# Optimization experiments

Measured on AMD Instinct MI355X. Metric: run time of the kernel, lower is better.

## Reference

```python
import jax, jax.numpy as jnp
import numpy as np

MAGBIAS = 0.01
INV_SQRT2 = np.float32(1.0 / np.sqrt(2.0))


def _reflect(x, minx, maxx):
    # Half-sample symmetric reflection of indices (static numpy; matches dtcwt reflect()).
    rng = maxx - minx
    mod = np.fmod(x - minx, 2.0 * rng)
    mod = np.where(mod < 0, mod + 2.0 * rng, mod)
    out = np.where(mod >= rng, 2.0 * rng - mod, mod) + minx
    return np.round(out).astype(np.int64)


def _symm_pad(l, m):
    return _reflect(np.arange(-m, l + m, dtype=np.float64), -0.5, l - 0.5)


def _depthwise(X, h, axis, stride):
    # Per-channel 1-D correlation along rows (axis=2) or cols (axis=3), NCHW, like F.conv2d(groups=ch).
    ch = X.shape[1]
    if axis == 2:
        k = h.reshape(1, 1, -1, 1)
        strides = (stride, 1)
    else:
        k = h.reshape(1, 1, 1, -1)
        strides = (1, stride)
    k = jnp.tile(k, (ch, 1, 1, 1)).astype(X.dtype)
    return jax.lax.conv_general_dilated(
        X, k, window_strides=strides, padding='VALID',
        dimension_numbers=('NCHW', 'OIHW', 'NCHW'), feature_group_count=ch)


def colfilter(X, h):
    m = h.shape[0] // 2
    xe = _symm_pad(X.shape[2], m)
    return _depthwise(X[:, :, xe, :], h, axis=2, stride=1)


def rowfilter(X, h):
    m = h.shape[0] // 2
    xe = _symm_pad(X.shape[3], m)
    return _depthwise(X[:, :, :, xe], h, axis=3, stride=1)


def coldfilt(X, ha, hb, highpass):
    # Dual-tree decimated column filtering with a quarter-shift pair; output rows = r // 2.
    b, ch, r, c = X.shape
    m = ha.shape[0]
    xe = _symm_pad(r, m)
    ya = _depthwise(X[:, :, xe[2::2], :], ha, axis=2, stride=2)  # (b,ch,r/4,c)
    yb = _depthwise(X[:, :, xe[3::2], :], hb, axis=2, stride=2)
    first, second = (yb, ya) if highpass else (ya, yb)
    return jnp.stack([first, second], axis=3).reshape(b, ch, r // 2, c)


def rowdfilt(X, ha, hb, highpass):
    b, ch, r, c = X.shape
    m = ha.shape[0]
    xe = _symm_pad(c, m)
    ya = _depthwise(X[:, :, :, xe[2::2]], ha, axis=3, stride=2)
    yb = _depthwise(X[:, :, :, xe[3::2]], hb, axis=3, stride=2)
    first, second = (yb, ya) if highpass else (ya, yb)
    return jnp.stack([first, second], axis=4).reshape(b, ch, r, c // 2)


def q2c(y):
    # Quads -> two complex subbands (real, imag): the DTCWT butterfly combine.
    y = y * INV_SQRT2
    a = y[..., 0::2, 0::2]
    b = y[..., 0::2, 1::2]
    c = y[..., 1::2, 0::2]
    d = y[..., 1::2, 1::2]
    return (a - d, b + c), (a + d, b - c)


def _stack_orients(lh, hl, hh):
    (d15r, d15i), (d165r, d165i) = q2c(lh)
    (d45r, d45i), (d135r, d135i) = q2c(hh)
    (d75r, d75i), (d105r, d105i) = q2c(hl)
    reals = jnp.stack([d15r, d45r, d75r, d105r, d135r, d165r], axis=1)
    imags = jnp.stack([d15i, d45i, d75i, d105i, d135i, d165i], axis=1)
    return reals, imags


def fwd_j1(x, h0, h1):
    # Level-1 DTCWT: undecimated separable biorthogonal filters + q2c.
    lo = rowfilter(x, h0)
    hi = rowfilter(x, h1)
    ll = colfilter(lo, h0)
    lh = colfilter(lo, h1)
    hl = colfilter(hi, h0)
    hh = colfilter(hi, h1)
    reals, imags = _stack_orients(lh, hl, hh)
    return ll, reals, imags


def fwd_j2plus(x, h0a, h1a, h0b, h1b):
    # Level-2 DTCWT: decimated quarter-shift filter pairs + q2c.
    lo = rowdfilt(x, h0b, h0a, False)
    hi = rowdfilt(x, h1b, h1a, True)
    ll = coldfilt(lo, h0b, h0a, False)
    lh = coldfilt(lo, h1b, h1a, True)
    hl = coldfilt(hi, h0b, h0a, False)
    hh = coldfilt(hi, h1b, h1a, True)
    reals, imags = _stack_orients(lh, hl, hh)
    return ll, reals, imags


def _smooth_mag(re, im, bias):
    return jnp.sqrt(re * re + im * im + bias * bias) - bias


def _avgpool2(x):
    b, ch, r, c = x.shape
    return x.reshape(b, ch, r // 2, 2, c // 2, 2).mean(axis=(3, 5))


def _scat_forward(x, h0o, h1o, h0a, h0b, h1a, h1b):
    b, ch, r, c = x.shape  # r, c multiples of 8 (input already padded)
    # First order, scale j=1
    ll, re, im = fwd_j1(x, h0o, h1o)
    s1_j1 = _smooth_mag(re, im, MAGBIAS)                      # (b,6,ch,r/2,c/2)
    # First order, scale j=2 (on the running lowpass)
    ll, re, im = fwd_j2plus(ll, h0a, h1a, h0b, h1b)           # ll: (b,ch,r/2,c/2)
    s1_j2 = _smooth_mag(re, im, MAGBIAS)                      # (b,6,ch,r/4,c/4)
    # Second order: one more octave on the first-order magnitudes
    p = s1_j1.reshape(b, 6 * ch, r // 2, c // 2)
    p, re, im = fwd_j1(p, h0o, h1o)
    s2 = _smooth_mag(re, im, MAGBIAS).reshape(b, 36, ch, r // 4, c // 4)
    s0 = _avgpool2(ll)[:, None]                               # (b,1,ch,r/4,c/4)
    s1_j1 = _avgpool2(p).reshape(b, 6, ch, r // 4, c // 4)
    Z = jnp.concatenate([s0, s1_j1, s1_j2, s2], axis=1)       # (b,49,ch,r/4,c/4)
    return Z.reshape(b, 49 * ch, r // 4, c // 4)


def setup_inputs():
    key = jax.random.key(0)
    ks = jax.random.split(key, 5)
    x = jax.random.normal(ks[0], (32, 3, 512, 512), dtype=jnp.float32)
    h0o = jax.random.normal(ks[1], (5,), dtype=jnp.float32) * 0.3
    h1o = jax.random.normal(ks[2], (7,), dtype=jnp.float32) * 0.3
    h0a = jax.random.normal(ks[3], (10,), dtype=jnp.float32) * 0.3
    h1a = jax.random.normal(ks[4], (10,), dtype=jnp.float32) * 0.3
    h0b = h0a[::-1]  # quarter-shift pair: time-reverse of the tree-a filter
    h1b = h1a[::-1]
    return {"x": x, "h0o": h0o, "h1o": h1o, "h0a": h0a, "h0b": h0b,
            "h1a": h1a, "h1b": h1b}


def reference(x, h0o, h1o, h0a, h0b, h1a, h1b):
    return _scat_forward(x, h0o, h1o, h0a, h0b, h1a, h1b)
```

## Files before the change

kernel.cpp:

```cpp
#include <hip/hip_runtime.h>

#define IS2 0.70710678118654752440f

__device__ __forceinline__ int refl(int i, int n) {
    if (i < 0) i = -1 - i;
    if (i >= n) i = 2 * n - 1 - i;
    return i;
}

__device__ __forceinline__ float smag(float re, float im) {
    return sqrtf(re * re + im * im + 1.0e-4f) - 0.01f;
}

template <int MODE>
__global__ __launch_bounds__(256, 4)
void fwd_j1_kernel(const float* __restrict__ in,
                   const float* __restrict__ h0,
                   const float* __restrict__ h1,
                   float* __restrict__ ll_out,
                   float* __restrict__ mag_out,
                   int CH, int N)
{
    const int img = blockIdx.z;
    const int b   = img / CH;
    const int chn = img % CH;
    const int ty0 = blockIdx.y * 64;
    const int tx0 = blockIdx.x * 64;
    const int tid = threadIdx.x;

    __shared__ __align__(16) float sx[70 * 72];
    __shared__ __align__(16) float slo[70 * 64];
    float* const shi = sx;

    float f0[5], f1[7];
#pragma unroll
    for (int t = 0; t < 5; ++t) f0[t] = h0[t];
#pragma unroll
    for (int t = 0; t < 7; ++t) f1[t] = h1[t];

    const float* src = in + (size_t)img * N * N;

    for (int e = tid; e < 70 * 70; e += 256) {
        int rr = e / 70, cc = e % 70;
        int gr = refl(ty0 - 3 + rr, N);
        int gc = refl(tx0 - 3 + cc, N);
        sx[rr * 72 + cc] = src[(size_t)gr * N + gc];
    }
    __syncthreads();

    float rlo[5][4], rhi[5][4];
#pragma unroll
    for (int k = 0; k < 5; ++k) {
        int e = tid + k * 256;
        if (e < 1120) {
            int rr = e >> 4, g = e & 15;
            const float4* w4 = (const float4*)&sx[rr * 72 + 4 * g];
            float4 wa = w4[0], wb = w4[1], wc = w4[2];
            float win[12] = {wa.x, wa.y, wa.z, wa.w,
                             wb.x, wb.y, wb.z, wb.w,
                             wc.x, wc.y, wc.z, wc.w};
#pragma unroll
            for (int u = 0; u < 4; ++u) {
                float lo = 0.f, hi = 0.f;
#pragma unroll
                for (int t = 0; t < 5; ++t) lo += win[u + 1 + t] * f0[t];
#pragma unroll
                for (int t = 0; t < 7; ++t) hi += win[u + t] * f1[t];
                rlo[k][u] = lo; rhi[k][u] = hi;
            }
        }
    }
    __syncthreads();
#pragma unroll
    for (int k = 0; k < 5; ++k) {
        int e = tid + k * 256;
        if (e < 1120) {
            int rr = e >> 4, g = e & 15;
            *(float4*)&slo[rr * 64 + 4 * g] =
                make_float4(rlo[k][0], rlo[k][1], rlo[k][2], rlo[k][3]);
            *(float4*)&shi[rr * 64 + 4 * g] =
                make_float4(rhi[k][0], rhi[k][1], rhi[k][2], rhi[k][3]);
        }
    }
    __syncthreads();

    const int j     = tid & 63;
    const int rg    = tid >> 6;
    const int rbase = rg * 16;

    float clo[22], chi[22];
#pragma unroll
    for (int t = 0; t < 22; ++t) {
        clo[t] = slo[(rbase + t) * 64 + j];
        chi[t] = shi[(rbase + t) * 64 + j];
    }

    const int Nh  = N >> 1;
    const int par = j & 1;
    const int qx  = (tx0 >> 1) + (j >> 1);
    const int qy0 = (ty0 >> 1) + rg * 8;
    const int oLH = par ? 5 : 0;
    const int oHH = par ? 4 : 1;
    const int oHL = par ? 3 : 2;

    float* lcol = nullptr;
    float* pLH = nullptr; float* pHH = nullptr; float* pHL = nullptr;
    float* zBase = nullptr;
    size_t zLH = 0, zHH = 0, zHL = 0, zPL = 0;
    if (MODE == 0) {
        lcol = ll_out + (size_t)img * N * N + (size_t)(ty0 + rbase) * N + tx0 + j;
        const size_t planeSz = (size_t)Nh * Nh;
        const size_t qoff = (size_t)qy0 * Nh + qx;
        pLH = mag_out + ((size_t)(b * 6 + oLH) * CH + chn) * planeSz + qoff;
        pHH = mag_out + ((size_t)(b * 6 + oHH) * CH + chn) * planeSz + qoff;
        pHL = mag_out + ((size_t)(b * 6 + oHL) * CH + chn) * planeSz + qoff;
    } else {
        const int o1 = chn / 3, c3 = chn % 3;
        zBase = mag_out + (size_t)b * 147 * 16384 + (size_t)qy0 * 128 + qx;
        zLH = (size_t)((13 + oLH * 6 + o1) * 3 + c3) * 16384;
        zHH = (size_t)((13 + oHH * 6 + o1) * 3 + c3) * 16384;
        zHL = (size_t)((13 + oHL * 6 + o1) * 3 + c3) * 16384;
        zPL = (size_t)((1 + o1) * 3 + c3) * 16384;
    }

#pragma unroll
    for (int ii = 0; ii < 8; ++ii) {
        const int i0 = 2 * ii, i1 = 2 * ii + 1;
        float ll0 = 0.f, ll1 = 0.f, lh0 = 0.f, lh1 = 0.f;
        float hl0 = 0.f, hl1 = 0.f, hh0 = 0.f, hh1 = 0.f;
#pragma unroll
        for (int t = 0; t < 5; ++t) {
            ll0 += clo[i0 + 1 + t] * f0[t]; ll1 += clo[i1 + 1 + t] * f0[t];
            hl0 += chi[i0 + 1 + t] * f0[t]; hl1 += chi[i1 + 1 + t] * f0[t];
        }
#pragma unroll
        for (int t = 0; t < 7; ++t) {
            lh0 += clo[i0 + t] * f1[t]; lh1 += clo[i1 + t] * f1[t];
            hh0 += chi[i0 + t] * f1[t]; hh1 += chi[i1 + t] * f1[t];
        }

        float lhT = __shfl_xor(lh0, 1), lhB = __shfl_xor(lh1, 1);
        float hhT = __shfl_xor(hh0, 1), hhB = __shfl_xor(hh1, 1);
        float hlT = __shfl_xor(hl0, 1), hlB = __shfl_xor(hl1, 1);
        float mLH = smag(IS2 * (lh0 - lhB), IS2 * (lhT + lh1));
        float mHH = smag(IS2 * (hh0 - hhB), IS2 * (hhT + hh1));
        float mHL = smag(IS2 * (hl0 - hlB), IS2 * (hlT + hl1));

        if (MODE == 0) {
            lcol[(size_t)i0 * N] = ll0;
            lcol[(size_t)i1 * N] = ll1;
            pLH[(size_t)ii * Nh] = mLH;
            pHH[(size_t)ii * Nh] = mHH;
            pHL[(size_t)ii * Nh] = mHL;
        } else {
            float* zr = zBase + (size_t)ii * 128;
            zr[zLH] = mLH;
            zr[zHH] = mHH;
            zr[zHL] = mHL;
            float llT = __shfl_xor(ll0, 1), llB = __shfl_xor(ll1, 1);
            if (par == 0) {
                zr[zPL] = 0.25f * (ll0 + ll1 + llT + llB);
            }
        }
    }
}

__global__ __launch_bounds__(256, 4)
void fwd_j2_kernel(const float* __restrict__ ll,
                   const float* __restrict__ h0a, const float* __restrict__ h0b,
                   const float* __restrict__ h1a, const float* __restrict__ h1b,
                   float* __restrict__ Z)
{
    const int img = blockIdx.z;
    const int b = img / 3, c = img % 3;
    const int r0 = blockIdx.y * 32;
    const int c0 = blockIdx.x * 32;
    const int tid = threadIdx.x;

    __shared__ float sx[80 * 84];
    float* const sloP = sx;
    float* const shiP = sx + 2688;

    float fa0[10], fb0[10], fa1[10], fb1[10];
#pragma unroll
    for (int t = 0; t < 10; ++t) {
        fa0[t] = h0a[t]; fb0[t] = h0b[t];
        fa1[t] = h1a[t]; fb1[t] = h1b[t];
    }

    const float* src = ll + (size_t)img * 512 * 512;

    for (int e = tid; e < 80 * 80; e += 256) {
        int rr = e / 80, cc = e % 80;
        int gr = refl(2 * r0 - 8 + rr, 512);
        int gc = refl(2 * c0 - 8 + cc, 512);
        sx[rr * 84 + cc] = src[(size_t)gr * 512 + gc];
    }
    __syncthreads();

    const int jj  = tid & 31;
    const int odd = jj & 1;
    const int base = 2 * (jj & ~1);
    float hlo[10], hhi[10];
#pragma unroll
    for (int t = 0; t < 10; ++t) {
        hlo[t] = odd ? fa0[t] : fb0[t];
        hhi[t] = odd ? fb1[t] : fa1[t];
    }
    const int offlo = base + odd;
    const int offhi = base + 1 - odd;
    float rlo[10], rhi[10];
#pragma unroll
    for (int k = 0; k < 10; ++k) {
        int rr = (tid >> 5) + 8 * k;
        const float* row = &sx[rr * 84];
        float lo = 0.f, hi = 0.f;
#pragma unroll
        for (int t = 0; t < 10; ++t) {
            lo += row[offlo + 2 * t] * hlo[t];
            hi += row[offhi + 2 * t] * hhi[t];
        }
        rlo[k] = lo; rhi[k] = hi;
    }
    __syncthreads();
#pragma unroll
    for (int k = 0; k < 10; ++k) {
        int rr = (tid >> 5) + 8 * k;
        sloP[rr * 33 + jj] = rlo[k];
        shiP[rr * 33 + jj] = rhi[k];
    }
    __syncthreads();

    const int qi = tid >> 4, qj = tid & 15;
    float ll2[2][2], lh4[2][2], hl4[2][2], hh4[2][2];
#pragma unroll
    for (int dj = 0; dj < 2; ++dj) {
        const int col = 2 * qj + dj;
        const int rb  = 4 * qi;
        float vll0 = 0.f, vll1 = 0.f, vlh0 = 0.f, vlh1 = 0.f;
        float vhl0 = 0.f, vhl1 = 0.f, vhh0 = 0.f, vhh1 = 0.f;
#pragma unroll
        for (int t = 0; t < 10; ++t) {
            float e0 = sloP[(rb + 2 * t) * 33 + col];
            float e1 = sloP[(rb + 2 * t + 1) * 33 + col];
            float g0 = shiP[(rb + 2 * t) * 33 + col];
            float g1 = shiP[(rb + 2 * t + 1) * 33 + col];
            vll0 += e0 * fb0[t];
            vll1 += e1 * fa0[t];
            vlh0 += e1 * fa1[t];
            vlh1 += e0 * fb1[t];
            vhl0 += g0 * fb0[t];
            vhl1 += g1 * fa0[t];
            vhh0 += g1 * fa1[t];
            vhh1 += g0 * fb1[t];
        }
        ll2[0][dj] = vll0; ll2[1][dj] = vll1;
        lh4[0][dj] = vlh0; lh4[1][dj] = vlh1;
        hl4[0][dj] = vhl0; hl4[1][dj] = vhl1;
        hh4[0][dj] = vhh0; hh4[1][dj] = vhh1;
    }

    const int qy = (r0 >> 1) + qi;
    const int qx = (c0 >> 1) + qj;
    float* Zb = Z + (size_t)b * 147 * 16384 + (size_t)qy * 128 + qx;

    Zb[(size_t)c * 16384] =
        0.25f * (ll2[0][0] + ll2[0][1] + ll2[1][0] + ll2[1][1]);

    {
        float a, bq, cq, d;
        float m[6];
        a = lh4[0][0] * IS2; bq = lh4[0][1] * IS2; cq = lh4[1][0] * IS2; d = lh4[1][1] * IS2;
        m[0] = smag(a - d, bq + cq); m[5] = smag(a + d, bq - cq);
        a = hh4[0][0] * IS2; bq = hh4[0][1] * IS2; cq = hh4[1][0] * IS2; d = hh4[1][1] * IS2;
        m[1] = smag(a - d, bq + cq); m[4] = smag(a + d, bq - cq);
        a = hl4[0][0] * IS2; bq = hl4[0][1] * IS2; cq = hl4[1][0] * IS2; d = hl4[1][1] * IS2;
        m[2] = smag(a - d, bq + cq); m[3] = smag(a + d, bq - cq);
#pragma unroll
        for (int o = 0; o < 6; ++o) {
            Zb[(size_t)((7 + o) * 3 + c) * 16384] = m[o];
        }
    }
}

extern "C" void kernel_launch(void* const* d_in, const int* in_sizes, int n_in,
                              void* d_out, int out_size, void* d_ws, size_t ws_size,
                              hipStream_t stream)
{
    const float* x   = (const float*)d_in[0];
    const float* h0o = (const float*)d_in[1];
    const float* h1o = (const float*)d_in[2];
    const float* h0a = (const float*)d_in[3];
    const float* h0b = (const float*)d_in[4];
    const float* h1a = (const float*)d_in[5];
    const float* h1b = (const float*)d_in[6];
    float* Z = (float*)d_out;

    float* ws_ll = (float*)d_ws;
    float* ws_p  = ws_ll + (size_t)32 * 3 * 512 * 512;

    dim3 blk(256);
    fwd_j1_kernel<0><<<dim3(8, 8, 96), blk, 0, stream>>>(x, h0o, h1o, ws_ll, ws_p, 3, 512);
    fwd_j2_kernel<<<dim3(8, 8, 96), blk, 0, stream>>>(ws_ll, h0a, h0b, h1a, h1b, Z);
    fwd_j1_kernel<1><<<dim3(4, 4, 576), blk, 0, stream>>>(ws_p, h0o, h1o, nullptr, Z, 18, 256);
}
```

Baseline: 630.3 us.

## Merge second-level and j1-on-magnitudes kernels into one launch

```diff
diff --git a/kernel.cpp b/kernel.cpp
--- a/kernel.cpp
+++ b/kernel.cpp
@@ -13,23 +13,21 @@
 }
 
 template <int MODE>
-__global__ __launch_bounds__(256, 4)
-void fwd_j1_kernel(const float* __restrict__ in,
-                   const float* __restrict__ h0,
-                   const float* __restrict__ h1,
-                   float* __restrict__ ll_out,
-                   float* __restrict__ mag_out,
-                   int CH, int N)
-{
-    const int img = blockIdx.z;
+__device__ __forceinline__
+void j1_tile(float* __restrict__ smem,
+             const float* __restrict__ in,
+             const float* __restrict__ h0,
+             const float* __restrict__ h1,
+             float* __restrict__ ll_out,
+             float* __restrict__ mag_out,
+             int CH, int N, int img, int ty0, int tx0)
+{
     const int b   = img / CH;
     const int chn = img % CH;
-    const int ty0 = blockIdx.y * 64;
-    const int tx0 = blockIdx.x * 64;
     const int tid = threadIdx.x;
 
-    __shared__ __align__(16) float sx[70 * 72];
-    __shared__ __align__(16) float slo[70 * 64];
+    float* const sx  = smem;
+    float* const slo = smem + 5040;
     float* const shi = sx;
 
     float f0[5], f1[7];
@@ -165,19 +163,17 @@
     }
 }
 
-__global__ __launch_bounds__(256, 4)
-void fwd_j2_kernel(const float* __restrict__ ll,
-                   const float* __restrict__ h0a, const float* __restrict__ h0b,
-                   const float* __restrict__ h1a, const float* __restrict__ h1b,
-                   float* __restrict__ Z)
-{
-    const int img = blockIdx.z;
+__device__ __forceinline__
+void j2_tile(float* __restrict__ smem,
+             const float* __restrict__ ll,
+             const float* __restrict__ h0a, const float* __restrict__ h0b,
+             const float* __restrict__ h1a, const float* __restrict__ h1b,
+             float* __restrict__ Z, int img, int r0, int c0)
+{
     const int b = img / 3, c = img % 3;
-    const int r0 = blockIdx.y * 32;
-    const int c0 = blockIdx.x * 32;
     const int tid = threadIdx.x;
 
-    __shared__ float sx[80 * 84];
+    float* const sx   = smem;
     float* const sloP = sx;
     float* const shiP = sx + 2688;
 
@@ -283,6 +279,37 @@
     }
 }
 
+__global__ __launch_bounds__(256, 4)
+void k_j1_l1(const float* __restrict__ x,
+             const float* __restrict__ h0o, const float* __restrict__ h1o,
+             float* __restrict__ ll, float* __restrict__ p)
+{
+    __shared__ __align__(16) float smem[9520];
+    j1_tile<0>(smem, x, h0o, h1o, ll, p, 3, 512,
+               blockIdx.z, blockIdx.y * 64, blockIdx.x * 64);
+}
+
+__global__ __launch_bounds__(256, 4)
+void k_p23(const float* __restrict__ ll, const float* __restrict__ p,
+           const float* __restrict__ h0o, const float* __restrict__ h1o,
+           const float* __restrict__ h0a, const float* __restrict__ h0b,
+           const float* __restrict__ h1a, const float* __restrict__ h1b,
+           float* __restrict__ Z)
+{
+    __shared__ __align__(16) float smem[9520];
+    const int B = blockIdx.x;
+    if (B < 6144) {
+        const int img = B >> 6, rem = B & 63;
+        j2_tile(smem, ll, h0a, h0b, h1a, h1b, Z,
+                img, ((rem >> 3) & 7) * 32, (rem & 7) * 32);
+    } else {
+        const int T = B - 6144;
+        const int img = T >> 4, rem = T & 15;
+        j1_tile<1>(smem, p, h0o, h1o, nullptr, Z, 18, 256,
+                   img, ((rem >> 2) & 3) * 64, (rem & 3) * 64);
+    }
+}
+
 extern "C" void kernel_launch(void* const* d_in, const int* in_sizes, int n_in,
                               void* d_out, int out_size, void* d_ws, size_t ws_size,
                               hipStream_t stream)
@@ -300,7 +327,7 @@
     float* ws_p  = ws_ll + (size_t)32 * 3 * 512 * 512;
 
     dim3 blk(256);
-    fwd_j1_kernel<0><<<dim3(8, 8, 96), blk, 0, stream>>>(x, h0o, h1o, ws_ll, ws_p, 3, 512);
-    fwd_j2_kernel<<<dim3(8, 8, 96), blk, 0, stream>>>(ws_ll, h0a, h0b, h1a, h1b, Z);
-    fwd_j1_kernel<1><<<dim3(4, 4, 576), blk, 0, stream>>>(ws_p, h0o, h1o, nullptr, Z, 18, 256);
-}
+    k_j1_l1<<<dim3(8, 8, 96), blk, 0, stream>>>(x, h0o, h1o, ws_ll, ws_p);
+    k_p23<<<dim3(15360), blk, 0, stream>>>(ws_ll, ws_p, h0o, h1o,
+                                           h0a, h0b, h1a, h1b, Z);
+}
```

New measurement: 590.3 us. 6.3% less time.
